# Kernel optimization log

Hardware: AMD Instinct MI355X
Metric: run time of the kernel (lower is better)

Reference implementation:

```python
import jax, jax.numpy as jnp
import numpy as np

B, H, S, D = 2, 12, 2048, 64
NEG = -1000000.0  # value used by masked_fill_ in the original


def setup_inputs() -> dict:
    key = jax.random.key(0)
    kq, kk, kv = jax.random.split(key, 3)
    q = jax.random.normal(kq, (B, H, S, D), dtype=jnp.float32)
    k = jax.random.normal(kk, (B, H, S, D), dtype=jnp.float32)
    # NOTE: original does attention_score * v ELEMENTWISE, so v has score shape
    v = jax.random.normal(kv, (B, H, S, S), dtype=jnp.float32)
    # causal mask: True = masked (upper triangle), broadcastable over B,H
    mask = jnp.triu(jnp.ones((S, S), dtype=bool), k=1)[None, None, :, :]
    return {"q": q, "k": k, "v": v, "mask": mask}


def reference(q, k, v, mask):
    d_k = q.shape[3]
    # scores: [B,H,Sq,Sk] = q @ k^T / sqrt(d_k)
    score = jnp.einsum("bhqd,bhkd->bhqk", q, k) / jnp.sqrt(jnp.asarray(d_k, q.dtype))
    score = jnp.where(mask, jnp.asarray(NEG, score.dtype), score)
    attn = jax.nn.softmax(score, axis=-1)
    out = attn * v  # elementwise, faithful to original
    return (out, attn)
```

## Files before the change

kernel.cpp:

```cpp
#include <hip/hip_runtime.h>
#include <cmath>


#define SDIM 2048
#define DDIM 64
#define BH 24
#define NT 128
#define PITCH 260

typedef __attribute__((ext_vector_type(8))) short short8_t;
typedef __attribute__((ext_vector_type(4))) float f32x4;

__device__ __forceinline__ unsigned short bf16_rne(float x) {
  unsigned int u = __float_as_uint(x);
  return (unsigned short)((u + 0x7FFFu + ((u >> 16) & 1u)) >> 16);
}

__global__ __launch_bounds__(256)
void prep_kfrag(const float* __restrict__ k, unsigned short* __restrict__ khi,
                unsigned short* __restrict__ klo) {
  const int lane = threadIdx.x & 63;
  const int blk  = blockIdx.x;
  const int wblk = (blk >> 3) + (blk & 7) * 192;
  const int gid  = wblk * 4 + (threadIdx.x >> 6);
  const int m2   = gid & 1;
  const int tile = (gid >> 1) & (NT - 1);
  const int bh   = gid >> 8;
  const int row  = 16 * tile + (lane & 15);
  const int d0   = 32 * m2 + 8 * (lane >> 4);
  const float* src = k + ((size_t)bh * SDIM + row) * DDIM + d0;
  f32x4 x0 = *(const f32x4*)(src);
  f32x4 x1 = *(const f32x4*)(src + 4);
  float x[8] = {x0[0], x0[1], x0[2], x0[3], x1[0], x1[1], x1[2], x1[3]};
  unsigned int hw[4], lw[4];
#pragma unroll
  for (int p = 0; p < 4; ++p) {
    unsigned short h0 = bf16_rne(x[2 * p]);
    unsigned short h1 = bf16_rne(x[2 * p + 1]);
    float f0 = __uint_as_float((unsigned int)h0 << 16);
    float f1 = __uint_as_float((unsigned int)h1 << 16);
    unsigned short l0 = bf16_rne(x[2 * p] - f0);
    unsigned short l1 = bf16_rne(x[2 * p + 1] - f1);
    hw[p] = (unsigned int)h0 | ((unsigned int)h1 << 16);
    lw[p] = (unsigned int)l0 | ((unsigned int)l1 << 16);
  }
  ((uint4*)(khi + (size_t)gid * 512))[lane] = make_uint4(hw[0], hw[1], hw[2], hw[3]);
  ((uint4*)(klo + (size_t)gid * 512))[lane] = make_uint4(lw[0], lw[1], lw[2], lw[3]);
}

__global__ __launch_bounds__(512, 4)
void qkv_attn_v6(const float* __restrict__ q, const float* __restrict__ v,
                 const unsigned short* __restrict__ khi,
                 const unsigned short* __restrict__ klo,
                 float* __restrict__ outp, float* __restrict__ attnp) {
  __shared__ float s_lds[2][16][PITCH];

  const int tid  = threadIdx.x;
  const int wave = tid >> 6;
  const int lane = tid & 63;

  const int blk  = blockIdx.x;
  const int wgid = (blk & 7) * 384 + (blk >> 3);
  const int bh   = wgid >> 7;
  const int t    = 127 - (wgid & 127);
  const int gmax = t >> 4;

  const int row0 = 16 * t + 2 * wave;
  const int row1 = row0 + 1;
  const size_t ob0 = ((size_t)bh * SDIM + row0) * SDIM;
  const size_t ob1 = ob0 + SDIM;
  const f32x4 zero4 = {0.f, 0.f, 0.f, 0.f};

#pragma unroll
  for (int g = 0; g < 8; ++g) {
    if (g > gmax) {
      const int coff = 256 * g + 4 * lane;
      __builtin_nontemporal_store(zero4, (f32x4*)(attnp + ob0 + coff));
      __builtin_nontemporal_store(zero4, (f32x4*)(attnp + ob1 + coff));
      __builtin_nontemporal_store(zero4, (f32x4*)(outp + ob0 + coff));
      __builtin_nontemporal_store(zero4, (f32x4*)(outp + ob1 + coff));
    }
  }

  short8_t qh[2], ql[2];
  {
    const int qrow = 16 * t + (lane & 15);
    const float* qp = q + ((size_t)bh * SDIM + qrow) * DDIM + 8 * (lane >> 4);
#pragma unroll
    for (int m2 = 0; m2 < 2; ++m2) {
      f32x4 x0 = *(const f32x4*)(qp + 32 * m2);
      f32x4 x1 = *(const f32x4*)(qp + 32 * m2 + 4);
      float x[8] = {x0[0], x0[1], x0[2], x0[3], x1[0], x1[1], x1[2], x1[3]};
#pragma unroll
      for (int j = 0; j < 8; ++j) {
        unsigned short hb = bf16_rne(x[j]);
        float hf = __uint_as_float((unsigned int)hb << 16);
        unsigned short lb = bf16_rne(x[j] - hf);
        qh[m2][j] = (short)hb;
        ql[m2][j] = (short)lb;
      }
    }
  }

  const short8_t* khb = (const short8_t*)khi + (size_t)bh * 16384 + lane;
  const short8_t* klb = (const short8_t*)klo + (size_t)bh * 16384 + lane;

  float sc[8][2][4];

#pragma unroll
  for (int ci = 0; ci < 8; ++ci) {
    if (ci <= gmax) {
      const int buf = ci & 1;
#pragma unroll
      for (int half = 0; half < 2; ++half) {
        const int ct = 16 * ci + 8 * half + wave;
        f32x4 acc;
        if (ct <= t) {
          const size_t off = (size_t)(2 * ct) * 64;
          short8_t kh0 = khb[off], kh1 = khb[off + 64];
          short8_t kl0 = klb[off], kl1 = klb[off + 64];
          acc = __builtin_amdgcn_mfma_f32_16x16x32_bf16(kh0, qh[0], zero4, 0, 0, 0);
          acc = __builtin_amdgcn_mfma_f32_16x16x32_bf16(kh1, qh[1], acc, 0, 0, 0);
          acc = __builtin_amdgcn_mfma_f32_16x16x32_bf16(kl0, qh[0], acc, 0, 0, 0);
          acc = __builtin_amdgcn_mfma_f32_16x16x32_bf16(kl1, qh[1], acc, 0, 0, 0);
          acc = __builtin_amdgcn_mfma_f32_16x16x32_bf16(kh0, ql[0], acc, 0, 0, 0);
          acc = __builtin_amdgcn_mfma_f32_16x16x32_bf16(kh1, ql[1], acc, 0, 0, 0);
        } else {
          acc = zero4;
        }
        *(f32x4*)&s_lds[buf][lane & 15][16 * wave + 128 * half + 4 * (lane >> 4)] = acc;
      }
      __syncthreads();
      const f32x4 r0v = *(const f32x4*)&s_lds[buf][2 * wave][4 * lane];
      const f32x4 r1v = *(const f32x4*)&s_lds[buf][2 * wave + 1][4 * lane];
      sc[ci][0][0] = r0v[0]; sc[ci][0][1] = r0v[1];
      sc[ci][0][2] = r0v[2]; sc[ci][0][3] = r0v[3];
      sc[ci][1][0] = r1v[0]; sc[ci][1][1] = r1v[1];
      sc[ci][1][2] = r1v[2]; sc[ci][1][3] = r1v[3];
    }
  }

  float l0 = 0.f, l1 = 0.f;
#pragma unroll
  for (int g = 0; g < 8; ++g) {
    if (g < gmax) {
#pragma unroll
      for (int e = 0; e < 4; ++e) {
        const float p0 = __expf(sc[g][0][e] * 0.125f);
        const float p1 = __expf(sc[g][1][e] * 0.125f);
        sc[g][0][e] = p0;  l0 += p0;
        sc[g][1][e] = p1;  l1 += p1;
      }
    } else if (g == gmax) {
#pragma unroll
      for (int e = 0; e < 4; ++e) {
        const int col = 256 * g + 4 * lane + e;
        const float p0 = (col <= row0) ? __expf(sc[g][0][e] * 0.125f) : 0.f;
        const float p1 = (col <= row1) ? __expf(sc[g][1][e] * 0.125f) : 0.f;
        sc[g][0][e] = p0;  l0 += p0;
        sc[g][1][e] = p1;  l1 += p1;
      }
    }
  }
#pragma unroll
  for (int off = 32; off > 0; off >>= 1) {
    l0 += __shfl_xor(l0, off, 64);
    l1 += __shfl_xor(l1, off, 64);
  }
  const float rl0 = 1.0f / l0;
  const float rl1 = 1.0f / l1;

#pragma unroll
  for (int g = 0; g < 8; ++g) {
    if (g <= gmax) {
      const int coff = 256 * g + 4 * lane;
      const f32x4 v0 = __builtin_nontemporal_load((const f32x4*)(v + ob0 + coff));
      const f32x4 v1 = __builtin_nontemporal_load((const f32x4*)(v + ob1 + coff));
      f32x4 a0, a1;
      a0[0] = sc[g][0][0] * rl0;  a0[1] = sc[g][0][1] * rl0;
      a0[2] = sc[g][0][2] * rl0;  a0[3] = sc[g][0][3] * rl0;
      a1[0] = sc[g][1][0] * rl1;  a1[1] = sc[g][1][1] * rl1;
      a1[2] = sc[g][1][2] * rl1;  a1[3] = sc[g][1][3] * rl1;
      __builtin_nontemporal_store(a0, (f32x4*)(attnp + ob0 + coff));
      __builtin_nontemporal_store(a1, (f32x4*)(attnp + ob1 + coff));
      __builtin_nontemporal_store(a0 * v0, (f32x4*)(outp + ob0 + coff));
      __builtin_nontemporal_store(a1 * v1, (f32x4*)(outp + ob1 + coff));
    }
  }
}

extern "C" void kernel_launch(void* const* d_in, const int* in_sizes, int n_in,
                              void* d_out, int out_size, void* d_ws, size_t ws_size,
                              hipStream_t stream) {
  const float* q = (const float*)d_in[0];
  const float* k = (const float*)d_in[1];
  const float* v = (const float*)d_in[2];
  float* outp  = (float*)d_out;
  float* attnp = outp + (size_t)BH * SDIM * SDIM;

  unsigned short* khi = (unsigned short*)d_ws;
  unsigned short* klo = khi + (size_t)BH * NT * 2 * 512;

  prep_kfrag<<<dim3(BH * NT * 2 / 4), dim3(256), 0, stream>>>(k, khi, klo);
  qkv_attn_v6<<<dim3(BH * NT), dim3(512), 0, stream>>>(q, v, khi, klo, outp, attnp);
}
```

Before: 218.8 us.

## Drop K low-part split in bf16x3 scores and batch V loads

Removes the low-order bf16 part of K, so the score product uses Khi*(Qhi+Qlo) instead of three split terms. This halves the K fragment traffic and removes two MFMAs per tile. The epilogue now issues up to eight V loads before the corresponding stores, giving more memory-level parallelism. The trade is reduced accuracy in the scores and higher register pressure from the batched loads.

Result: faster. 209.0 us (-4.5%).

```diff
diff --git a/kernel.cpp b/kernel.cpp
--- a/kernel.cpp
+++ b/kernel.cpp
@@ -17,8 +17,7 @@
 }
 
 __global__ __launch_bounds__(256)
-void prep_kfrag(const float* __restrict__ k, unsigned short* __restrict__ khi,
-                unsigned short* __restrict__ klo) {
+void prep_kfrag(const float* __restrict__ k, unsigned short* __restrict__ khi) {
   const int lane = threadIdx.x & 63;
   const int blk  = blockIdx.x;
   const int wblk = (blk >> 3) + (blk & 7) * 192;
@@ -32,26 +31,19 @@
   f32x4 x0 = *(const f32x4*)(src);
   f32x4 x1 = *(const f32x4*)(src + 4);
   float x[8] = {x0[0], x0[1], x0[2], x0[3], x1[0], x1[1], x1[2], x1[3]};
-  unsigned int hw[4], lw[4];
+  unsigned int hw[4];
 #pragma unroll
   for (int p = 0; p < 4; ++p) {
     unsigned short h0 = bf16_rne(x[2 * p]);
     unsigned short h1 = bf16_rne(x[2 * p + 1]);
-    float f0 = __uint_as_float((unsigned int)h0 << 16);
-    float f1 = __uint_as_float((unsigned int)h1 << 16);
-    unsigned short l0 = bf16_rne(x[2 * p] - f0);
-    unsigned short l1 = bf16_rne(x[2 * p + 1] - f1);
     hw[p] = (unsigned int)h0 | ((unsigned int)h1 << 16);
-    lw[p] = (unsigned int)l0 | ((unsigned int)l1 << 16);
   }
   ((uint4*)(khi + (size_t)gid * 512))[lane] = make_uint4(hw[0], hw[1], hw[2], hw[3]);
-  ((uint4*)(klo + (size_t)gid * 512))[lane] = make_uint4(lw[0], lw[1], lw[2], lw[3]);
 }
 
 __global__ __launch_bounds__(512, 4)
-void qkv_attn_v6(const float* __restrict__ q, const float* __restrict__ v,
+void qkv_attn_v7(const float* __restrict__ q, const float* __restrict__ v,
                  const unsigned short* __restrict__ khi,
-                 const unsigned short* __restrict__ klo,
                  float* __restrict__ outp, float* __restrict__ attnp) {
   __shared__ float s_lds[2][16][PITCH];
 
@@ -103,7 +95,6 @@
   }
 
   const short8_t* khb = (const short8_t*)khi + (size_t)bh * 16384 + lane;
-  const short8_t* klb = (const short8_t*)klo + (size_t)bh * 16384 + lane;
 
   float sc[8][2][4];
 
@@ -118,11 +109,8 @@
         if (ct <= t) {
           const size_t off = (size_t)(2 * ct) * 64;
           short8_t kh0 = khb[off], kh1 = khb[off + 64];
-          short8_t kl0 = klb[off], kl1 = klb[off + 64];
           acc = __builtin_amdgcn_mfma_f32_16x16x32_bf16(kh0, qh[0], zero4, 0, 0, 0);
           acc = __builtin_amdgcn_mfma_f32_16x16x32_bf16(kh1, qh[1], acc, 0, 0, 0);
-          acc = __builtin_amdgcn_mfma_f32_16x16x32_bf16(kl0, qh[0], acc, 0, 0, 0);
-          acc = __builtin_amdgcn_mfma_f32_16x16x32_bf16(kl1, qh[1], acc, 0, 0, 0);
           acc = __builtin_amdgcn_mfma_f32_16x16x32_bf16(kh0, ql[0], acc, 0, 0, 0);
           acc = __builtin_amdgcn_mfma_f32_16x16x32_bf16(kh1, ql[1], acc, 0, 0, 0);
         } else {
@@ -171,20 +159,32 @@
   const float rl1 = 1.0f / l1;
 
 #pragma unroll
-  for (int g = 0; g < 8; ++g) {
-    if (g <= gmax) {
-      const int coff = 256 * g + 4 * lane;
-      const f32x4 v0 = __builtin_nontemporal_load((const f32x4*)(v + ob0 + coff));
-      const f32x4 v1 = __builtin_nontemporal_load((const f32x4*)(v + ob1 + coff));
-      f32x4 a0, a1;
-      a0[0] = sc[g][0][0] * rl0;  a0[1] = sc[g][0][1] * rl0;
-      a0[2] = sc[g][0][2] * rl0;  a0[3] = sc[g][0][3] * rl0;
-      a1[0] = sc[g][1][0] * rl1;  a1[1] = sc[g][1][1] * rl1;
-      a1[2] = sc[g][1][2] * rl1;  a1[3] = sc[g][1][3] * rl1;
-      __builtin_nontemporal_store(a0, (f32x4*)(attnp + ob0 + coff));
-      __builtin_nontemporal_store(a1, (f32x4*)(attnp + ob1 + coff));
-      __builtin_nontemporal_store(a0 * v0, (f32x4*)(outp + ob0 + coff));
-      __builtin_nontemporal_store(a1 * v1, (f32x4*)(outp + ob1 + coff));
+  for (int gb = 0; gb < 2; ++gb) {
+    f32x4 vv0[4], vv1[4];
+#pragma unroll
+    for (int i = 0; i < 4; ++i) {
+      const int g = 4 * gb + i;
+      if (g <= gmax) {
+        const int coff = 256 * g + 4 * lane;
+        vv0[i] = __builtin_nontemporal_load((const f32x4*)(v + ob0 + coff));
+        vv1[i] = __builtin_nontemporal_load((const f32x4*)(v + ob1 + coff));
+      }
+    }
+#pragma unroll
+    for (int i = 0; i < 4; ++i) {
+      const int g = 4 * gb + i;
+      if (g <= gmax) {
+        const int coff = 256 * g + 4 * lane;
+        f32x4 a0, a1;
+        a0[0] = sc[g][0][0] * rl0;  a0[1] = sc[g][0][1] * rl0;
+        a0[2] = sc[g][0][2] * rl0;  a0[3] = sc[g][0][3] * rl0;
+        a1[0] = sc[g][1][0] * rl1;  a1[1] = sc[g][1][1] * rl1;
+        a1[2] = sc[g][1][2] * rl1;  a1[3] = sc[g][1][3] * rl1;
+        __builtin_nontemporal_store(a0, (f32x4*)(attnp + ob0 + coff));
+        __builtin_nontemporal_store(a1, (f32x4*)(attnp + ob1 + coff));
+        __builtin_nontemporal_store(a0 * vv0[i], (f32x4*)(outp + ob0 + coff));
+        __builtin_nontemporal_store(a1 * vv1[i], (f32x4*)(outp + ob1 + coff));
+      }
     }
   }
 }
@@ -199,8 +199,7 @@
   float* attnp = outp + (size_t)BH * SDIM * SDIM;
 
   unsigned short* khi = (unsigned short*)d_ws;
-  unsigned short* klo = khi + (size_t)BH * NT * 2 * 512;
-
-  prep_kfrag<<<dim3(BH * NT * 2 / 4), dim3(256), 0, stream>>>(k, khi, klo);
-  qkv_attn_v6<<<dim3(BH * NT), dim3(512), 0, stream>>>(q, v, khi, klo, outp, attnp);
-}
+
+  prep_kfrag<<<dim3(BH * NT * 2 / 4), dim3(256), 0, stream>>>(k, khi);
+  qkv_attn_v7<<<dim3(BH * NT), dim3(512), 0, stream>>>(q, v, khi, outp, attnp);
+}
```
